# Kernel optimization log

Measured on AMD Instinct MI355X. Metric: run time of the kernel, lower is better.

Reference implementation:

```python
import jax, jax.numpy as jnp
import numpy as np

HIDDEN = 2048
INTER = 1408
N_ROUTED = 32
N_SHARED = 2
TOP_K = 6
B, S = 2, 1024


def setup_inputs() -> dict:
    key = jax.random.key(0)
    ks = jax.random.split(key, 9)
    scale = 0.02
    x = jax.random.normal(ks[0], (B, S, HIDDEN), dtype=jnp.float32)
    w_router = jax.random.normal(ks[1], (HIDDEN, N_ROUTED), dtype=jnp.float32) * scale
    wg = jax.random.normal(ks[2], (N_ROUTED, HIDDEN, INTER), dtype=jnp.float32) * scale
    wu = jax.random.normal(ks[3], (N_ROUTED, HIDDEN, INTER), dtype=jnp.float32) * scale
    wd = jax.random.normal(ks[4], (N_ROUTED, INTER, HIDDEN), dtype=jnp.float32) * scale
    sg = jax.random.normal(ks[5], (N_SHARED, HIDDEN, INTER), dtype=jnp.float32) * scale
    su = jax.random.normal(ks[6], (N_SHARED, HIDDEN, INTER), dtype=jnp.float32) * scale
    sd = jax.random.normal(ks[7], (N_SHARED, INTER, HIDDEN), dtype=jnp.float32) * scale
    return {"x": x, "w_router": w_router, "wg": wg, "wu": wu, "wd": wd,
            "sg": sg, "su": su, "sd": sd}


def _swiglu(xf, wg_e, wu_e, wd_e):
    # xf: [T, D]; wg_e/wu_e: [D, F]; wd_e: [F, D]
    h = jax.nn.silu(xf @ wg_e) * (xf @ wu_e)
    return h @ wd_e


def reference(x, w_router, wg, wu, wd, sg, su, sd):
    Bb, Ss, D = x.shape
    xf = x.reshape(-1, D)                      # [T, D], T = B*S
    T = xf.shape[0]

    # Shared experts: applied densely to every token, summed.
    shared = jnp.zeros_like(xf)
    for i in range(sg.shape[0]):               # small fixed count (2)
        shared = shared + _swiglu(xf, sg[i], su[i], sd[i])

    # Router: softmax over all routed experts, then top-k + renormalize.
    probs = jax.nn.softmax(xf @ w_router, axis=-1)            # [T, E]
    topw, topi = jax.lax.top_k(probs, TOP_K)                  # [T, K]
    topw = topw / jnp.sum(topw, axis=-1, keepdims=True)

    # Dense [T, E] combine weights (zero where expert not selected).
    E = wg.shape[0]
    wdense = jnp.zeros((T, E), dtype=xf.dtype)
    wdense = wdense.at[jnp.arange(T)[:, None], topi].add(topw)

    # Scan over experts, accumulating weighted expert outputs (memory-light).
    def body(acc, ew):
        wg_e, wu_e, wd_e, w_e = ew            # w_e: [T] combine weight for this expert
        y = _swiglu(xf, wg_e, wu_e, wd_e)     # [T, D]
        return acc + w_e[:, None] * y, None

    routed, _ = jax.lax.scan(body, jnp.zeros_like(xf), (wg, wu, wd, wdense.T))

    return (shared + routed).reshape(Bb, Ss, D)
```

## Files before the change

kernel.cpp:

```cpp
#include <hip/hip_runtime.h>
#include <hip/hip_bf16.h>

#define T_TOK 2048
#define D_HID 2048
#define F_INT 1408
#define N_EXP 32
#define TOPK 6
#define NJOBS 34
#define SH_BASE 12288
#define ROWS_TOTAL 16384
#define MAXT_GU 288
#define MAXT_DN 159
#define LDSW 40

typedef __bf16 bf16;
typedef __bf16 bf16x4 __attribute__((ext_vector_type(4)));
typedef __bf16 bf16x8 __attribute__((ext_vector_type(8)));
typedef float f32x4 __attribute__((ext_vector_type(4)));

#define BAR() asm volatile("s_waitcnt lgkmcnt(0)\n\ts_barrier" ::: "memory")

__device__ __forceinline__ int swz16(int r, int k) {
    return r * LDSW + (((k >> 3) ^ ((r >> 3) & 3)) << 3) + (k & 7);
}

__device__ __forceinline__ int decode_tile(const int* __restrict__ counts, int bid,
                                           int NBN, int MSH, int NSH,
                                           int& job, int& n0, int& m0) {
    int total = 0;
    for (int j = 0; j < NJOBS; ++j) {
        int c = (j < N_EXP) ? counts[j] : T_TOK;
        total += ((c + (1 << MSH) - 1) >> MSH) * NBN;
    }
    if (bid >= total) return 0;
    int q = total >> 3, r = total & 7, x = bid & 7, o = bid >> 3;
    int L = (x < r ? x * (q + 1) : r * (q + 1) + (x - r) * q) + o;
    int acc = 0;
    for (int j = 0; j < NJOBS; ++j) {
        int c = (j < N_EXP) ? counts[j] : T_TOK;
        int tc = (c + (1 << MSH) - 1) >> MSH;
        int b = tc * NBN;
        if (L < acc + b) {
            int rem = L - acc;
            int n0i = rem / tc;
            job = j;
            n0 = n0i << NSH;
            m0 = (rem - n0i * tc) << MSH;
            return 1;
        }
        acc += b;
    }
    return 0;
}

__global__ __launch_bounds__(256) void k_xcvt(const float* __restrict__ x,
                                              bf16* __restrict__ xb) {
    int i = blockIdx.x * 2048 + threadIdx.x * 8;
    float4 f0 = *(const float4*)(x + i);
    float4 f1 = *(const float4*)(x + i + 4);
    bf16x8 v = {(bf16)f0.x, (bf16)f0.y, (bf16)f0.z, (bf16)f0.w,
                (bf16)f1.x, (bf16)f1.y, (bf16)f1.z, (bf16)f1.w};
    *(bf16x8*)(xb + i) = v;
}

__global__ __launch_bounds__(256) void k_router(const float* __restrict__ x,
                                                const float* __restrict__ wr,
                                                int* __restrict__ counts,
                                                int* __restrict__ tok_e,
                                                float* __restrict__ tok_w) {
    int t = blockIdx.x;
    int tid = threadIdx.x;
    __shared__ float xs[D_HID];
    __shared__ float part[8][32];
    __shared__ float probs[N_EXP];

    const float4* xsrc = (const float4*)(x + (size_t)t * D_HID);
    float4* xdst = (float4*)xs;
    for (int i = tid; i < D_HID / 4; i += 256) xdst[i] = xsrc[i];
    __syncthreads();

    int e = tid & 31, c = tid >> 5;
    float p = 0.f;
    const float* wp = wr + e;
    #pragma unroll 8
    for (int h = c * 256; h < c * 256 + 256; ++h) p += xs[h] * wp[h * 32];
    part[c][e] = p;
    __syncthreads();

    if (tid < 32) {
        float l = 0.f;
        #pragma unroll
        for (int cc = 0; cc < 8; ++cc) l += part[cc][tid];
        float m = l;
        for (int off = 16; off; off >>= 1) m = fmaxf(m, __shfl_xor(m, off));
        float ex = __expf(l - m);
        float s = ex;
        for (int off = 16; off; off >>= 1) s += __shfl_xor(s, off);
        probs[tid] = ex / s;
    }
    __syncthreads();

    if (tid == 0) {
        unsigned used = 0;
        int ids[TOPK]; float wsv[TOPK]; float wsum = 0.f;
        for (int k = 0; k < TOPK; ++k) {
            int best = 0; float bv = -1.f;
            for (int ee = 0; ee < N_EXP; ++ee)
                if (!((used >> ee) & 1u) && probs[ee] > bv) { bv = probs[ee]; best = ee; }
            used |= 1u << best;
            ids[k] = best; wsv[k] = bv; wsum += bv;
        }
        float inv = 1.f / wsum;
        for (int k = 0; k < TOPK; ++k) {
            tok_e[t * TOPK + k] = ids[k];
            tok_w[t * TOPK + k] = wsv[k] * inv;
            atomicAdd(&counts[ids[k]], 1);
        }
    }
}

__global__ void k_plan(const int* __restrict__ counts, int* __restrict__ offs,
                       int* __restrict__ cursors) {
    int tid = threadIdx.x;
    if (tid < N_EXP) cursors[tid] = 0;
    if (tid == 0) {
        int o = 0;
        offs[0] = 0;
        for (int e2 = 0; e2 < N_EXP; ++e2) { o += counts[e2]; offs[e2 + 1] = o; }
        offs[33] = offs[32] + T_TOK;
        offs[34] = offs[33] + T_TOK;
    }
}

__global__ __launch_bounds__(256) void k_assign(const int* __restrict__ tok_e,
                                                const int* __restrict__ offs,
                                                int* __restrict__ cursors,
                                                int* __restrict__ slots,
                                                int* __restrict__ rowtok) {
    int t = blockIdx.x * 256 + threadIdx.x;
    #pragma unroll
    for (int k = 0; k < TOPK; ++k) {
        int e = tok_e[t * TOPK + k];
        int pos = atomicAdd(&cursors[e], 1);
        int slot = offs[e] + pos;
        slots[t * TOPK + k] = slot;
        rowtok[slot] = t;
    }
    rowtok[SH_BASE + t] = t;
    rowtok[SH_BASE + T_TOK + t] = t;
}

__global__ __launch_bounds__(256, 3) void k_gateup(
    const bf16* __restrict__ xb, const float* __restrict__ wg, const float* __restrict__ wu,
    const float* __restrict__ sg, const float* __restrict__ su,
    const int* __restrict__ rowtok, const int* __restrict__ counts, const int* __restrict__ offs,
    bf16* __restrict__ H) {

    int job, n0, m0;
    if (!decode_tile(counts, blockIdx.x, F_INT / 128, 6, 7, job, n0, m0)) return;
    int cnt = (job < N_EXP) ? counts[job] : T_TOK;
    int base = offs[job];
    const float* Wg = (job < N_EXP) ? wg + (size_t)job * D_HID * F_INT
                                    : sg + (size_t)(job - N_EXP) * D_HID * F_INT;
    const float* Wu = (job < N_EXP) ? wu + (size_t)job * D_HID * F_INT
                                    : su + (size_t)(job - N_EXP) * D_HID * F_INT;

    __shared__ bf16 As[2][64 * LDSW];
    __shared__ bf16 Bg[2][128 * LDSW];
    __shared__ bf16 Bu[2][128 * LDSW];

    int tid = threadIdx.x;
    int lane = tid & 63;
    int wid = tid >> 6;
    int wm = (wid >> 1) * 32;
    int wn = (wid & 1) * 64;

    int ar = tid >> 2;
    int akg = tid & 3;
    int grow_a = m0 + ar; if (grow_a > cnt - 1) grow_a = cnt - 1;
    const bf16* asrc = xb + (size_t)rowtok[base + grow_a] * D_HID + akg * 8;

    int k4 = (tid >> 5) * 4;
    int nn = (tid & 31) * 4;
    const float* gsrc = Wg + (size_t)k4 * F_INT + n0 + nn;
    const float* usrc = Wu + (size_t)k4 * F_INT + n0 + nn;

    f32x4 accg[2][4], accu[2][4];
    f32x4 zero = {0.f, 0.f, 0.f, 0.f};
    #pragma unroll
    for (int i = 0; i < 2; ++i)
        #pragma unroll
        for (int j = 0; j < 4; ++j) { accg[i][j] = zero; accu[i][j] = zero; }

    bf16x8 a_r8;
    float4 g_r[4], u_r[4];

    auto LOAD = [&](int k0) {
        a_r8 = *(const bf16x8*)(asrc + k0);
        const float* g0 = gsrc + (size_t)k0 * F_INT;
        g_r[0] = *(const float4*)g0;
        g_r[1] = *(const float4*)(g0 + F_INT);
        g_r[2] = *(const float4*)(g0 + 2 * F_INT);
        g_r[3] = *(const float4*)(g0 + 3 * F_INT);
        const float* u0 = usrc + (size_t)k0 * F_INT;
        u_r[0] = *(const float4*)u0;
        u_r[1] = *(const float4*)(u0 + F_INT);
        u_r[2] = *(const float4*)(u0 + 2 * F_INT);
        u_r[3] = *(const float4*)(u0 + 3 * F_INT);
    };

    auto WRITE = [&](int s) {
        *(bf16x8*)&As[s][swz16(ar, akg * 8)] = a_r8;
        bf16x4 p0 = {(bf16)g_r[0].x, (bf16)g_r[1].x, (bf16)g_r[2].x, (bf16)g_r[3].x};
        bf16x4 p1 = {(bf16)g_r[0].y, (bf16)g_r[1].y, (bf16)g_r[2].y, (bf16)g_r[3].y};
        bf16x4 p2 = {(bf16)g_r[0].z, (bf16)g_r[1].z, (bf16)g_r[2].z, (bf16)g_r[3].z};
        bf16x4 p3 = {(bf16)g_r[0].w, (bf16)g_r[1].w, (bf16)g_r[2].w, (bf16)g_r[3].w};
        *(bf16x4*)&Bg[s][swz16(nn + 0, k4)] = p0;
        *(bf16x4*)&Bg[s][swz16(nn + 1, k4)] = p1;
        *(bf16x4*)&Bg[s][swz16(nn + 2, k4)] = p2;
        *(bf16x4*)&Bg[s][swz16(nn + 3, k4)] = p3;
        bf16x4 q0 = {(bf16)u_r[0].x, (bf16)u_r[1].x, (bf16)u_r[2].x, (bf16)u_r[3].x};
        bf16x4 q1 = {(bf16)u_r[0].y, (bf16)u_r[1].y, (bf16)u_r[2].y, (bf16)u_r[3].y};
        bf16x4 q2 = {(bf16)u_r[0].z, (bf16)u_r[1].z, (bf16)u_r[2].z, (bf16)u_r[3].z};
        bf16x4 q3 = {(bf16)u_r[0].w, (bf16)u_r[1].w, (bf16)u_r[2].w, (bf16)u_r[3].w};
        *(bf16x4*)&Bu[s][swz16(nn + 0, k4)] = q0;
        *(bf16x4*)&Bu[s][swz16(nn + 1, k4)] = q1;
        *(bf16x4*)&Bu[s][swz16(nn + 2, k4)] = q2;
        *(bf16x4*)&Bu[s][swz16(nn + 3, k4)] = q3;
    };

    const int NT = D_HID / 32;
    LOAD(0);
    WRITE(0);
    LOAD(32);
    BAR();

    for (int kt = 0; kt < NT; ++kt) {
        int cur = kt & 1;
        if (kt + 1 < NT) WRITE(cur ^ 1);
        if (kt + 2 < NT) LOAD((kt + 2) * 32);

        int kgl = (lane >> 4) * 8;
        bf16x8 af[2];
        #pragma unroll
        for (int mf = 0; mf < 2; ++mf)
            af[mf] = *(const bf16x8*)&As[cur][swz16(wm + mf * 16 + (lane & 15), kgl)];
        #pragma unroll
        for (int nf = 0; nf < 4; ++nf) {
            int rn = wn + nf * 16 + (lane & 15);
            bf16x8 bfr = *(const bf16x8*)&Bg[cur][swz16(rn, kgl)];
            bf16x8 ufr = *(const bf16x8*)&Bu[cur][swz16(rn, kgl)];
            #pragma unroll
            for (int mf = 0; mf < 2; ++mf) {
                accg[mf][nf] = __builtin_amdgcn_mfma_f32_16x16x32_bf16(af[mf], bfr, accg[mf][nf], 0, 0, 0);
                accu[mf][nf] = __builtin_amdgcn_mfma_f32_16x16x32_bf16(af[mf], ufr, accu[mf][nf], 0, 0, 0);
            }
        }
        BAR();
    }

    #pragma unroll
    for (int mf = 0; mf < 2; ++mf) {
        #pragma unroll
        for (int nf = 0; nf < 4; ++nf) {
            int col = n0 + wn + nf * 16 + (lane & 15);
            #pragma unroll
            for (int r = 0; r < 4; ++r) {
                int grow = m0 + wm + mf * 16 + (lane >> 4) * 4 + r;
                if (grow < cnt) {
                    float g = accg[mf][nf][r];
                    float u = accu[mf][nf][r];
                    float h = g * u / (1.f + __expf(-g));
                    H[(size_t)(base + grow) * F_INT + col] = (bf16)h;
                }
            }
        }
    }
}

__global__ __launch_bounds__(256, 3) void k_down(
    const bf16* __restrict__ H, const float* __restrict__ wd, const float* __restrict__ sd,
    const int* __restrict__ counts, const int* __restrict__ offs,
    bf16* __restrict__ P) {

    int job, n0, m0;
    if (!decode_tile(counts, blockIdx.x, D_HID / 128, 7, 7, job, n0, m0)) return;
    int cnt = (job < N_EXP) ? counts[job] : T_TOK;
    int base = offs[job];
    const float* Wd = (job < N_EXP) ? wd + (size_t)job * F_INT * D_HID
                                    : sd + (size_t)(job - N_EXP) * F_INT * D_HID;

    __shared__ bf16 As[2][128 * LDSW];
    __shared__ bf16 Bs[2][128 * LDSW];

    int tid = threadIdx.x;
    int lane = tid & 63;
    int wid = tid >> 6;
    int wm = (wid >> 1) * 64;
    int wn = (wid & 1) * 64;

    int ar = tid >> 1;
    int akg2 = (tid & 1) * 2;
    int grow_a = m0 + ar; if (grow_a > cnt - 1) grow_a = cnt - 1;
    const bf16* asrc = H + (size_t)(base + grow_a) * F_INT + akg2 * 8;

    int k4 = (tid >> 5) * 4;
    int nn = (tid & 31) * 4;
    const float* bsrc = Wd + (size_t)k4 * D_HID + n0 + nn;

    f32x4 acc[4][4];
    f32x4 zero = {0.f, 0.f, 0.f, 0.f};
    #pragma unroll
    for (int i = 0; i < 4; ++i)
        #pragma unroll
        for (int j = 0; j < 4; ++j) acc[i][j] = zero;

    bf16x8 h_r[2];
    float4 b_r[4];

    auto LOAD = [&](int k0) {
        h_r[0] = *(const bf16x8*)(asrc + k0);
        h_r[1] = *(const bf16x8*)(asrc + k0 + 8);
        const float* b0 = bsrc + (size_t)k0 * D_HID;
        b_r[0] = *(const float4*)b0;
        b_r[1] = *(const float4*)(b0 + D_HID);
        b_r[2] = *(const float4*)(b0 + 2 * D_HID);
        b_r[3] = *(const float4*)(b0 + 3 * D_HID);
    };

    auto WRITE = [&](int s) {
        *(bf16x8*)&As[s][swz16(ar, akg2 * 8)] = h_r[0];
        *(bf16x8*)&As[s][swz16(ar, (akg2 + 1) * 8)] = h_r[1];
        bf16x4 p0 = {(bf16)b_r[0].x, (bf16)b_r[1].x, (bf16)b_r[2].x, (bf16)b_r[3].x};
        bf16x4 p1 = {(bf16)b_r[0].y, (bf16)b_r[1].y, (bf16)b_r[2].y, (bf16)b_r[3].y};
        bf16x4 p2 = {(bf16)b_r[0].z, (bf16)b_r[1].z, (bf16)b_r[2].z, (bf16)b_r[3].z};
        bf16x4 p3 = {(bf16)b_r[0].w, (bf16)b_r[1].w, (bf16)b_r[2].w, (bf16)b_r[3].w};
        *(bf16x4*)&Bs[s][swz16(nn + 0, k4)] = p0;
        *(bf16x4*)&Bs[s][swz16(nn + 1, k4)] = p1;
        *(bf16x4*)&Bs[s][swz16(nn + 2, k4)] = p2;
        *(bf16x4*)&Bs[s][swz16(nn + 3, k4)] = p3;
    };

    const int NT = F_INT / 32;
    LOAD(0);
    WRITE(0);
    LOAD(32);
    BAR();

    for (int kt = 0; kt < NT; ++kt) {
        int cur = kt & 1;
        if (kt + 1 < NT) WRITE(cur ^ 1);
        if (kt + 2 < NT) LOAD((kt + 2) * 32);

        int kgl = (lane >> 4) * 8;
        bf16x8 af[4];
        #pragma unroll
        for (int mf = 0; mf < 4; ++mf)
            af[mf] = *(const bf16x8*)&As[cur][swz16(wm + mf * 16 + (lane & 15), kgl)];
        #pragma unroll
        for (int nf = 0; nf < 4; ++nf) {
            int rn = wn + nf * 16 + (lane & 15);
            bf16x8 bfr = *(const bf16x8*)&Bs[cur][swz16(rn, kgl)];
            #pragma unroll
            for (int mf = 0; mf < 4; ++mf)
                acc[mf][nf] = __builtin_amdgcn_mfma_f32_16x16x32_bf16(af[mf], bfr, acc[mf][nf], 0, 0, 0);
        }
        BAR();
    }

    #pragma unroll
    for (int mf = 0; mf < 4; ++mf) {
        #pragma unroll
        for (int nf = 0; nf < 4; ++nf) {
            int col = n0 + wn + nf * 16 + (lane & 15);
            #pragma unroll
            for (int r = 0; r < 4; ++r) {
                int grow = m0 + wm + mf * 16 + (lane >> 4) * 4 + r;
                if (grow < cnt)
                    P[(size_t)(base + grow) * D_HID + col] = (bf16)acc[mf][nf][r];
            }
        }
    }
}

__global__ __launch_bounds__(256) void k_combine(const bf16* __restrict__ P,
                                                 const int* __restrict__ slots,
                                                 const float* __restrict__ tok_w,
                                                 float* __restrict__ out) {
    int t = blockIdx.x;
    int tid = threadIdx.x;
    __shared__ int ss[TOPK];
    __shared__ float ww[TOPK];
    if (tid < TOPK) { ss[tid] = slots[t * TOPK + tid]; ww[tid] = tok_w[t * TOPK + tid]; }
    __syncthreads();
    int c0 = tid * 8;
    float acc[8];
    {
        bf16x8 v0 = *(const bf16x8*)(P + (size_t)(SH_BASE + t) * D_HID + c0);
        bf16x8 v1 = *(const bf16x8*)(P + (size_t)(SH_BASE + T_TOK + t) * D_HID + c0);
        #pragma unroll
        for (int i = 0; i < 8; ++i) acc[i] = (float)v0[i] + (float)v1[i];
    }
    #pragma unroll
    for (int k = 0; k < TOPK; ++k) {
        bf16x8 v = *(const bf16x8*)(P + (size_t)ss[k] * D_HID + c0);
        float w = ww[k];
        #pragma unroll
        for (int i = 0; i < 8; ++i) acc[i] += w * (float)v[i];
    }
    float4 o0 = {acc[0], acc[1], acc[2], acc[3]};
    float4 o1 = {acc[4], acc[5], acc[6], acc[7]};
    *(float4*)(out + (size_t)t * D_HID + c0) = o0;
    *(float4*)(out + (size_t)t * D_HID + c0 + 4) = o1;
}

extern "C" void kernel_launch(void* const* d_in, const int* in_sizes, int n_in,
                              void* d_out, int out_size, void* d_ws, size_t ws_size,
                              hipStream_t stream) {
    const float* x  = (const float*)d_in[0];
    const float* wr = (const float*)d_in[1];
    const float* wg = (const float*)d_in[2];
    const float* wu = (const float*)d_in[3];
    const float* wd = (const float*)d_in[4];
    const float* sg = (const float*)d_in[5];
    const float* su = (const float*)d_in[6];
    const float* sd = (const float*)d_in[7];
    float* out = (float*)d_out;

    char* w = (char*)d_ws;
    int*   counts   = (int*)(w + 0);
    int*   cursors  = (int*)(w + 256);
    int*   offs     = (int*)(w + 512);
    int*   tok_e    = (int*)(w + 8192);
    float* tok_w    = (float*)(w + 8192 + 49152);
    int*   slots    = (int*)(w + 8192 + 2 * 49152);
    int*   rowtok   = (int*)(w + 8192 + 3 * 49152);
    bf16*  H        = (bf16*)(w + 262144);
    bf16*  P        = (bf16*)(w + 262144 + (size_t)ROWS_TOTAL * F_INT * 2);
    bf16*  Xb       = (bf16*)(w + 262144 + (size_t)ROWS_TOTAL * F_INT * 2
                                        + (size_t)ROWS_TOTAL * D_HID * 2);

    hipMemsetAsync(counts, 0, 128, stream);
    k_xcvt<<<T_TOK * D_HID / 2048, 256, 0, stream>>>(x, Xb);
    k_router<<<T_TOK, 256, 0, stream>>>(x, wr, counts, tok_e, tok_w);
    k_plan<<<1, 64, 0, stream>>>(counts, offs, cursors);
    k_assign<<<T_TOK / 256, 256, 0, stream>>>(tok_e, offs, cursors, slots, rowtok);
    k_gateup<<<MAXT_GU * (F_INT / 128), 256, 0, stream>>>(
        Xb, wg, wu, sg, su, rowtok, counts, offs, H);
    k_down<<<MAXT_DN * (D_HID / 128), 256, 0, stream>>>(
        H, wd, sd, counts, offs, P);
    k_combine<<<T_TOK, 256, 0, stream>>>(P, slots, tok_w, out);
}
```

Before: 777.1 us.

## Retile gate/up GEMM to 256-row tiles with gate/up wave specialization

```diff
diff --git a/kernel.cpp b/kernel.cpp
--- a/kernel.cpp
+++ b/kernel.cpp
@@ -9,7 +9,8 @@
 #define NJOBS 34
 #define SH_BASE 12288
 #define ROWS_TOTAL 16384
-#define MAXT_GU 288
+#define MAXT_GU 96
+#define GU_NBN 22
 #define MAXT_DN 159
 #define LDSW 40
 
@@ -24,13 +25,12 @@
     return r * LDSW + (((k >> 3) ^ ((r >> 3) & 3)) << 3) + (k & 7);
 }
 
-__device__ __forceinline__ int decode_tile(const int* __restrict__ counts, int bid,
-                                           int NBN, int MSH, int NSH,
-                                           int& job, int& n0, int& m0) {
+__device__ __forceinline__ int decode_gu(const int* __restrict__ counts, int bid,
+                                         int& job, int& n0, int& m0) {
     int total = 0;
     for (int j = 0; j < NJOBS; ++j) {
         int c = (j < N_EXP) ? counts[j] : T_TOK;
-        total += ((c + (1 << MSH) - 1) >> MSH) * NBN;
+        total += ((c + 255) >> 8) * GU_NBN;
     }
     if (bid >= total) return 0;
     int q = total >> 3, r = total & 7, x = bid & 7, o = bid >> 3;
@@ -38,14 +38,42 @@
     int acc = 0;
     for (int j = 0; j < NJOBS; ++j) {
         int c = (j < N_EXP) ? counts[j] : T_TOK;
-        int tc = (c + (1 << MSH) - 1) >> MSH;
+        int tc = (c + 255) >> 8;
+        int b = tc * GU_NBN;
+        if (L < acc + b) {
+            int rem = L - acc;
+            job = j;
+            m0 = (rem / GU_NBN) << 8;
+            n0 = (rem % GU_NBN) << 6;
+            return 1;
+        }
+        acc += b;
+    }
+    return 0;
+}
+
+__device__ __forceinline__ int decode_dn(const int* __restrict__ counts, int bid,
+                                         int& job, int& n0, int& m0) {
+    const int NBN = D_HID / 128;
+    int total = 0;
+    for (int j = 0; j < NJOBS; ++j) {
+        int c = (j < N_EXP) ? counts[j] : T_TOK;
+        total += ((c + 127) >> 7) * NBN;
+    }
+    if (bid >= total) return 0;
+    int q = total >> 3, r = total & 7, x = bid & 7, o = bid >> 3;
+    int L = (x < r ? x * (q + 1) : r * (q + 1) + (x - r) * q) + o;
+    int acc = 0;
+    for (int j = 0; j < NJOBS; ++j) {
+        int c = (j < N_EXP) ? counts[j] : T_TOK;
+        int tc = (c + 127) >> 7;
         int b = tc * NBN;
         if (L < acc + b) {
             int rem = L - acc;
             int n0i = rem / tc;
             job = j;
-            n0 = n0i << NSH;
-            m0 = (rem - n0i * tc) << MSH;
+            n0 = n0i << 7;
+            m0 = (rem - n0i * tc) << 7;
             return 1;
         }
         acc += b;
@@ -150,14 +178,14 @@
     rowtok[SH_BASE + T_TOK + t] = t;
 }
 
-__global__ __launch_bounds__(256, 3) void k_gateup(
+__global__ __launch_bounds__(512, 4) void k_gateup(
     const bf16* __restrict__ xb, const float* __restrict__ wg, const float* __restrict__ wu,
     const float* __restrict__ sg, const float* __restrict__ su,
     const int* __restrict__ rowtok, const int* __restrict__ counts, const int* __restrict__ offs,
     bf16* __restrict__ H) {
 
     int job, n0, m0;
-    if (!decode_tile(counts, blockIdx.x, F_INT / 128, 6, 7, job, n0, m0)) return;
+    if (!decode_gu(counts, blockIdx.x, job, n0, m0)) return;
     int cnt = (job < N_EXP) ? counts[job] : T_TOK;
     int base = offs[job];
     const float* Wg = (job < N_EXP) ? wg + (size_t)job * D_HID * F_INT
@@ -165,68 +193,68 @@
     const float* Wu = (job < N_EXP) ? wu + (size_t)job * D_HID * F_INT
                                     : su + (size_t)(job - N_EXP) * D_HID * F_INT;
 
-    __shared__ bf16 As[2][64 * LDSW];
-    __shared__ bf16 Bg[2][128 * LDSW];
-    __shared__ bf16 Bu[2][128 * LDSW];
+    __shared__ bf16 AsF[2 * 256 * LDSW];
+    __shared__ bf16 BgF[2 * 64 * LDSW];
+    __shared__ bf16 BuF[2 * 64 * LDSW];
 
     int tid = threadIdx.x;
     int lane = tid & 63;
     int wid = tid >> 6;
-    int wm = (wid >> 1) * 32;
-    int wn = (wid & 1) * 64;
-
-    int ar = tid >> 2;
-    int akg = tid & 3;
+    int mat = wid & 1;
+    int wm = (wid >> 1) * 64;
+
+    int bt  = tid & 127;
+    int kk  = (bt >> 4) * 4;
+    int nn  = (bt & 15) * 4;
+    const float* wsrc = ((wid < 2) ? Wg : Wu) + (size_t)kk * F_INT + n0 + nn;
+    bf16* bdst = (wid < 2) ? BgF : BuF;
+    int ar = tid & 255;
     int grow_a = m0 + ar; if (grow_a > cnt - 1) grow_a = cnt - 1;
-    const bf16* asrc = xb + (size_t)rowtok[base + grow_a] * D_HID + akg * 8;
-
-    int k4 = (tid >> 5) * 4;
-    int nn = (tid & 31) * 4;
-    const float* gsrc = Wg + (size_t)k4 * F_INT + n0 + nn;
-    const float* usrc = Wu + (size_t)k4 * F_INT + n0 + nn;
-
-    f32x4 accg[2][4], accu[2][4];
+    const bf16* asrc = xb + (size_t)rowtok[base + grow_a] * D_HID;
+
+    f32x4 acc[4][4];
     f32x4 zero = {0.f, 0.f, 0.f, 0.f};
     #pragma unroll
-    for (int i = 0; i < 2; ++i)
-        #pragma unroll
-        for (int j = 0; j < 4; ++j) { accg[i][j] = zero; accu[i][j] = zero; }
-
-    bf16x8 a_r8;
-    float4 g_r[4], u_r[4];
+    for (int i = 0; i < 4; ++i)
+        #pragma unroll
+        for (int j = 0; j < 4; ++j) acc[i][j] = zero;
+
+    float4 st[4];
 
     auto LOAD = [&](int k0) {
-        a_r8 = *(const bf16x8*)(asrc + k0);
-        const float* g0 = gsrc + (size_t)k0 * F_INT;
-        g_r[0] = *(const float4*)g0;
-        g_r[1] = *(const float4*)(g0 + F_INT);
-        g_r[2] = *(const float4*)(g0 + 2 * F_INT);
-        g_r[3] = *(const float4*)(g0 + 3 * F_INT);
-        const float* u0 = usrc + (size_t)k0 * F_INT;
-        u_r[0] = *(const float4*)u0;
-        u_r[1] = *(const float4*)(u0 + F_INT);
-        u_r[2] = *(const float4*)(u0 + 2 * F_INT);
-        u_r[3] = *(const float4*)(u0 + 3 * F_INT);
+        if (wid < 4) {
+            const float* s0 = wsrc + (size_t)k0 * F_INT;
+            st[0] = *(const float4*)s0;
+            st[1] = *(const float4*)(s0 + F_INT);
+            st[2] = *(const float4*)(s0 + 2 * F_INT);
+            st[3] = *(const float4*)(s0 + 3 * F_INT);
+        } else {
+            const bf16* a0 = asrc + k0;
+            st[0] = *(const float4*)(const void*)(a0);
+            st[1] = *(const float4*)(const void*)(a0 + 8);
+            st[2] = *(const float4*)(const void*)(a0 + 16);
+            st[3] = *(const float4*)(const void*)(a0 + 24);
+        }
     };
 
     auto WRITE = [&](int s) {
-        *(bf16x8*)&As[s][swz16(ar, akg * 8)] = a_r8;
-        bf16x4 p0 = {(bf16)g_r[0].x, (bf16)g_r[1].x, (bf16)g_r[2].x, (bf16)g_r[3].x};
-        bf16x4 p1 = {(bf16)g_r[0].y, (bf16)g_r[1].y, (bf16)g_r[2].y, (bf16)g_r[3].y};
-        bf16x4 p2 = {(bf16)g_r[0].z, (bf16)g_r[1].z, (bf16)g_r[2].z, (bf16)g_r[3].z};
-        bf16x4 p3 = {(bf16)g_r[0].w, (bf16)g_r[1].w, (bf16)g_r[2].w, (bf16)g_r[3].w};
-        *(bf16x4*)&Bg[s][swz16(nn + 0, k4)] = p0;
-        *(bf16x4*)&Bg[s][swz16(nn + 1, k4)] = p1;
-        *(bf16x4*)&Bg[s][swz16(nn + 2, k4)] = p2;
-        *(bf16x4*)&Bg[s][swz16(nn + 3, k4)] = p3;
-        bf16x4 q0 = {(bf16)u_r[0].x, (bf16)u_r[1].x, (bf16)u_r[2].x, (bf16)u_r[3].x};
-        bf16x4 q1 = {(bf16)u_r[0].y, (bf16)u_r[1].y, (bf16)u_r[2].y, (bf16)u_r[3].y};
-        bf16x4 q2 = {(bf16)u_r[0].z, (bf16)u_r[1].z, (bf16)u_r[2].z, (bf16)u_r[3].z};
-        bf16x4 q3 = {(bf16)u_r[0].w, (bf16)u_r[1].w, (bf16)u_r[2].w, (bf16)u_r[3].w};
-        *(bf16x4*)&Bu[s][swz16(nn + 0, k4)] = q0;
-        *(bf16x4*)&Bu[s][swz16(nn + 1, k4)] = q1;
-        *(bf16x4*)&Bu[s][swz16(nn + 2, k4)] = q2;
-        *(bf16x4*)&Bu[s][swz16(nn + 3, k4)] = q3;
+        if (wid < 4) {
+            bf16* bd = bdst + s * (64 * LDSW);
+            bf16x4 p0 = {(bf16)st[0].x, (bf16)st[1].x, (bf16)st[2].x, (bf16)st[3].x};
+            bf16x4 p1 = {(bf16)st[0].y, (bf16)st[1].y, (bf16)st[2].y, (bf16)st[3].y};
+            bf16x4 p2 = {(bf16)st[0].z, (bf16)st[1].z, (bf16)st[2].z, (bf16)st[3].z};
+            bf16x4 p3 = {(bf16)st[0].w, (bf16)st[1].w, (bf16)st[2].w, (bf16)st[3].w};
+            *(bf16x4*)&bd[swz16(nn + 0, kk)] = p0;
+            *(bf16x4*)&bd[swz16(nn + 1, kk)] = p1;
+            *(bf16x4*)&bd[swz16(nn + 2, kk)] = p2;
+            *(bf16x4*)&bd[swz16(nn + 3, kk)] = p3;
+        } else {
+            bf16* ad = AsF + s * (256 * LDSW);
+            *(float4*)(void*)&ad[swz16(ar, 0)]  = st[0];
+            *(float4*)(void*)&ad[swz16(ar, 8)]  = st[1];
+            *(float4*)(void*)&ad[swz16(ar, 16)] = st[2];
+            *(float4*)(void*)&ad[swz16(ar, 24)] = st[3];
+        }
     };
 
     const int NT = D_HID / 32;
@@ -235,46 +263,60 @@
     LOAD(32);
     BAR();
 
+    const bf16* bread = mat ? BuF : BgF;
     for (int kt = 0; kt < NT; ++kt) {
         int cur = kt & 1;
         if (kt + 1 < NT) WRITE(cur ^ 1);
         if (kt + 2 < NT) LOAD((kt + 2) * 32);
 
         int kgl = (lane >> 4) * 8;
-        bf16x8 af[2];
-        #pragma unroll
-        for (int mf = 0; mf < 2; ++mf)
-            af[mf] = *(const bf16x8*)&As[cur][swz16(wm + mf * 16 + (lane & 15), kgl)];
+        const bf16* ac = AsF + cur * (256 * LDSW);
+        const bf16* bc = bread + cur * (64 * LDSW);
+        bf16x8 af[4];
+        #pragma unroll
+        for (int mf = 0; mf < 4; ++mf)
+            af[mf] = *(const bf16x8*)&ac[swz16(wm + mf * 16 + (lane & 15), kgl)];
         #pragma unroll
         for (int nf = 0; nf < 4; ++nf) {
-            int rn = wn + nf * 16 + (lane & 15);
-            bf16x8 bfr = *(const bf16x8*)&Bg[cur][swz16(rn, kgl)];
-            bf16x8 ufr = *(const bf16x8*)&Bu[cur][swz16(rn, kgl)];
+            bf16x8 bfr = *(const bf16x8*)&bc[swz16(nf * 16 + (lane & 15), kgl)];
             #pragma unroll
-            for (int mf = 0; mf < 2; ++mf) {
-                accg[mf][nf] = __builtin_amdgcn_mfma_f32_16x16x32_bf16(af[mf], bfr, accg[mf][nf], 0, 0, 0);
-                accu[mf][nf] = __builtin_amdgcn_mfma_f32_16x16x32_bf16(af[mf], ufr, accu[mf][nf], 0, 0, 0);
-            }
+            for (int mf = 0; mf < 4; ++mf)
+                acc[mf][nf] = __builtin_amdgcn_mfma_f32_16x16x32_bf16(af[mf], bfr, acc[mf][nf], 0, 0, 0);
         }
         BAR();
     }
 
-    #pragma unroll
-    for (int mf = 0; mf < 2; ++mf) {
-        #pragma unroll
-        for (int nf = 0; nf < 4; ++nf) {
-            int col = n0 + wn + nf * 16 + (lane & 15);
+    bf16* uscr = AsF;
+    if (mat == 1) {
+        #pragma unroll
+        for (int mf = 0; mf < 4; ++mf)
             #pragma unroll
-            for (int r = 0; r < 4; ++r) {
-                int grow = m0 + wm + mf * 16 + (lane >> 4) * 4 + r;
-                if (grow < cnt) {
-                    float g = accg[mf][nf][r];
-                    float u = accu[mf][nf][r];
-                    float h = g * u / (1.f + __expf(-g));
-                    H[(size_t)(base + grow) * F_INT + col] = (bf16)h;
+            for (int nf = 0; nf < 4; ++nf)
+                #pragma unroll
+                for (int r = 0; r < 4; ++r) {
+                    int row = mf * 16 + (lane >> 4) * 4 + r;
+                    int col = nf * 16 + (lane & 15);
+                    uscr[(wm + row) * 64 + (col ^ ((row & 7) << 3))] = (bf16)acc[mf][nf][r];
                 }
-            }
-        }
+    }
+    __syncthreads();
+    if (mat == 0) {
+        #pragma unroll
+        for (int mf = 0; mf < 4; ++mf)
+            #pragma unroll
+            for (int nf = 0; nf < 4; ++nf)
+                #pragma unroll
+                for (int r = 0; r < 4; ++r) {
+                    int row = mf * 16 + (lane >> 4) * 4 + r;
+                    int col = nf * 16 + (lane & 15);
+                    int grow = m0 + wm + row;
+                    if (grow < cnt) {
+                        float u = (float)uscr[(wm + row) * 64 + (col ^ ((row & 7) << 3))];
+                        float g = acc[mf][nf][r];
+                        float h = g * u / (1.f + __expf(-g));
+                        H[(size_t)(base + grow) * F_INT + n0 + col] = (bf16)h;
+                    }
+                }
     }
 }
 
@@ -284,7 +326,7 @@
     bf16* __restrict__ P) {
 
     int job, n0, m0;
-    if (!decode_tile(counts, blockIdx.x, D_HID / 128, 7, 7, job, n0, m0)) return;
+    if (!decode_dn(counts, blockIdx.x, job, n0, m0)) return;
     int cnt = (job < N_EXP) ? counts[job] : T_TOK;
     int base = offs[job];
     const float* Wd = (job < N_EXP) ? wd + (size_t)job * F_INT * D_HID
@@ -445,7 +487,7 @@
     k_router<<<T_TOK, 256, 0, stream>>>(x, wr, counts, tok_e, tok_w);
     k_plan<<<1, 64, 0, stream>>>(counts, offs, cursors);
     k_assign<<<T_TOK / 256, 256, 0, stream>>>(tok_e, offs, cursors, slots, rowtok);
-    k_gateup<<<MAXT_GU * (F_INT / 128), 256, 0, stream>>>(
+    k_gateup<<<MAXT_GU * GU_NBN, 512, 0, stream>>>(
         Xb, wg, wu, sg, su, rowtok, counts, offs, H);
     k_down<<<MAXT_DN * (D_HID / 128), 256, 0, stream>>>(
         H, wd, sd, counts, offs, P);
```

After: 1.179 ms. +51.8%, slower.

## Reshape gate/up tile to 128 tokens by 64 columns and extend LDS swizzle

Applied to the files above, without the earlier changes.

```diff
diff --git a/kernel.cpp b/kernel.cpp
--- a/kernel.cpp
+++ b/kernel.cpp
@@ -9,7 +9,8 @@
 #define NJOBS 34
 #define SH_BASE 12288
 #define ROWS_TOTAL 16384
-#define MAXT_GU 288
+#define MAXT_GU 159
+#define GU_NBN 22
 #define MAXT_DN 159
 #define LDSW 40
 
@@ -21,7 +22,7 @@
 #define BAR() asm volatile("s_waitcnt lgkmcnt(0)\n\ts_barrier" ::: "memory")
 
 __device__ __forceinline__ int swz16(int r, int k) {
-    return r * LDSW + (((k >> 3) ^ ((r >> 3) & 3)) << 3) + (k & 7);
+    return r * LDSW + ((((k >> 3) ^ ((r >> 3) & 3) ^ ((r >> 5) & 3)) & 3) << 3) + (k & 7);
 }
 
 __device__ __forceinline__ int decode_tile(const int* __restrict__ counts, int bid,
@@ -157,7 +158,7 @@
     bf16* __restrict__ H) {
 
     int job, n0, m0;
-    if (!decode_tile(counts, blockIdx.x, F_INT / 128, 6, 7, job, n0, m0)) return;
+    if (!decode_tile(counts, blockIdx.x, GU_NBN, 7, 6, job, n0, m0)) return;
     int cnt = (job < N_EXP) ? counts[job] : T_TOK;
     int base = offs[job];
     const float* Wg = (job < N_EXP) ? wg + (size_t)job * D_HID * F_INT
@@ -165,68 +166,58 @@
     const float* Wu = (job < N_EXP) ? wu + (size_t)job * D_HID * F_INT
                                     : su + (size_t)(job - N_EXP) * D_HID * F_INT;
 
-    __shared__ bf16 As[2][64 * LDSW];
-    __shared__ bf16 Bg[2][128 * LDSW];
-    __shared__ bf16 Bu[2][128 * LDSW];
+    __shared__ bf16 As[2][128 * LDSW];
+    __shared__ bf16 Bg[2][64 * LDSW];
+    __shared__ bf16 Bu[2][64 * LDSW];
 
     int tid = threadIdx.x;
     int lane = tid & 63;
     int wid = tid >> 6;
-    int wm = (wid >> 1) * 32;
-    int wn = (wid & 1) * 64;
-
-    int ar = tid >> 2;
-    int akg = tid & 3;
+    int wm = (wid & 1) * 64;
+    int wn = (wid >> 1) * 32;
+
+    int ar = tid >> 1;
+    int akg2 = (tid & 1) * 2;
     int grow_a = m0 + ar; if (grow_a > cnt - 1) grow_a = cnt - 1;
-    const bf16* asrc = xb + (size_t)rowtok[base + grow_a] * D_HID + akg * 8;
-
-    int k4 = (tid >> 5) * 4;
-    int nn = (tid & 31) * 4;
-    const float* gsrc = Wg + (size_t)k4 * F_INT + n0 + nn;
-    const float* usrc = Wu + (size_t)k4 * F_INT + n0 + nn;
-
-    f32x4 accg[2][4], accu[2][4];
+    const bf16* asrc = xb + (size_t)rowtok[base + grow_a] * D_HID + akg2 * 8;
+
+    int sub = tid & 127;
+    int k4 = (sub & 7) * 4;
+    int nn = (sub >> 3) * 4;
+    const float* wsrc = ((tid & 128) ? Wu : Wg) + (size_t)k4 * F_INT + n0 + nn;
+
+    f32x4 accg[4][2], accu[4][2];
     f32x4 zero = {0.f, 0.f, 0.f, 0.f};
     #pragma unroll
-    for (int i = 0; i < 2; ++i)
-        #pragma unroll
-        for (int j = 0; j < 4; ++j) { accg[i][j] = zero; accu[i][j] = zero; }
-
-    bf16x8 a_r8;
-    float4 g_r[4], u_r[4];
+    for (int i = 0; i < 4; ++i)
+        #pragma unroll
+        for (int j = 0; j < 2; ++j) { accg[i][j] = zero; accu[i][j] = zero; }
+
+    bf16x8 a_r[2];
+    float4 b_r[4];
 
     auto LOAD = [&](int k0) {
-        a_r8 = *(const bf16x8*)(asrc + k0);
-        const float* g0 = gsrc + (size_t)k0 * F_INT;
-        g_r[0] = *(const float4*)g0;
-        g_r[1] = *(const float4*)(g0 + F_INT);
-        g_r[2] = *(const float4*)(g0 + 2 * F_INT);
-        g_r[3] = *(const float4*)(g0 + 3 * F_INT);
-        const float* u0 = usrc + (size_t)k0 * F_INT;
-        u_r[0] = *(const float4*)u0;
-        u_r[1] = *(const float4*)(u0 + F_INT);
-        u_r[2] = *(const float4*)(u0 + 2 * F_INT);
-        u_r[3] = *(const float4*)(u0 + 3 * F_INT);
+        a_r[0] = *(const bf16x8*)(asrc + k0);
+        a_r[1] = *(const bf16x8*)(asrc + k0 + 8);
+        const float* b0 = wsrc + (size_t)k0 * F_INT;
+        b_r[0] = *(const float4*)b0;
+        b_r[1] = *(const float4*)(b0 + F_INT);
+        b_r[2] = *(const float4*)(b0 + 2 * F_INT);
+        b_r[3] = *(const float4*)(b0 + 3 * F_INT);
     };
 
     auto WRITE = [&](int s) {
-        *(bf16x8*)&As[s][swz16(ar, akg * 8)] = a_r8;
-        bf16x4 p0 = {(bf16)g_r[0].x, (bf16)g_r[1].x, (bf16)g_r[2].x, (bf16)g_r[3].x};
-        bf16x4 p1 = {(bf16)g_r[0].y, (bf16)g_r[1].y, (bf16)g_r[2].y, (bf16)g_r[3].y};
-        bf16x4 p2 = {(bf16)g_r[0].z, (bf16)g_r[1].z, (bf16)g_r[2].z, (bf16)g_r[3].z};
-        bf16x4 p3 = {(bf16)g_r[0].w, (bf16)g_r[1].w, (bf16)g_r[2].w, (bf16)g_r[3].w};
-        *(bf16x4*)&Bg[s][swz16(nn + 0, k4)] = p0;
-        *(bf16x4*)&Bg[s][swz16(nn + 1, k4)] = p1;
-        *(bf16x4*)&Bg[s][swz16(nn + 2, k4)] = p2;
-        *(bf16x4*)&Bg[s][swz16(nn + 3, k4)] = p3;
-        bf16x4 q0 = {(bf16)u_r[0].x, (bf16)u_r[1].x, (bf16)u_r[2].x, (bf16)u_r[3].x};
-        bf16x4 q1 = {(bf16)u_r[0].y, (bf16)u_r[1].y, (bf16)u_r[2].y, (bf16)u_r[3].y};
-        bf16x4 q2 = {(bf16)u_r[0].z, (bf16)u_r[1].z, (bf16)u_r[2].z, (bf16)u_r[3].z};
-        bf16x4 q3 = {(bf16)u_r[0].w, (bf16)u_r[1].w, (bf16)u_r[2].w, (bf16)u_r[3].w};
-        *(bf16x4*)&Bu[s][swz16(nn + 0, k4)] = q0;
-        *(bf16x4*)&Bu[s][swz16(nn + 1, k4)] = q1;
-        *(bf16x4*)&Bu[s][swz16(nn + 2, k4)] = q2;
-        *(bf16x4*)&Bu[s][swz16(nn + 3, k4)] = q3;
+        *(bf16x8*)&As[s][swz16(ar, akg2 * 8)] = a_r[0];
+        *(bf16x8*)&As[s][swz16(ar, (akg2 + 1) * 8)] = a_r[1];
+        bf16* bd = (tid & 128) ? Bu[s] : Bg[s];
+        bf16x4 p0 = {(bf16)b_r[0].x, (bf16)b_r[1].x, (bf16)b_r[2].x, (bf16)b_r[3].x};
+        bf16x4 p1 = {(bf16)b_r[0].y, (bf16)b_r[1].y, (bf16)b_r[2].y, (bf16)b_r[3].y};
+        bf16x4 p2 = {(bf16)b_r[0].z, (bf16)b_r[1].z, (bf16)b_r[2].z, (bf16)b_r[3].z};
+        bf16x4 p3 = {(bf16)b_r[0].w, (bf16)b_r[1].w, (bf16)b_r[2].w, (bf16)b_r[3].w};
+        *(bf16x4*)&bd[swz16(nn + 0, k4)] = p0;
+        *(bf16x4*)&bd[swz16(nn + 1, k4)] = p1;
+        *(bf16x4*)&bd[swz16(nn + 2, k4)] = p2;
+        *(bf16x4*)&bd[swz16(nn + 3, k4)] = p3;
     };
 
     const int NT = D_HID / 32;
@@ -241,17 +232,18 @@
         if (kt + 2 < NT) LOAD((kt + 2) * 32);
 
         int kgl = (lane >> 4) * 8;
-        bf16x8 af[2];
-        #pragma unroll
-        for (int mf = 0; mf < 2; ++mf)
+        bf16x8 af[4];
+        #pragma unroll
+        for (int mf = 0; mf < 4; ++mf)
             af[mf] = *(const bf16x8*)&As[cur][swz16(wm + mf * 16 + (lane & 15), kgl)];
         #pragma unroll
-        for (int nf = 0; nf < 4; ++nf) {
+        for (int nf = 0; nf < 2; ++nf) {
             int rn = wn + nf * 16 + (lane & 15);
-            bf16x8 bfr = *(const bf16x8*)&Bg[cur][swz16(rn, kgl)];
-            bf16x8 ufr = *(const bf16x8*)&Bu[cur][swz16(rn, kgl)];
+            int o = swz16(rn, kgl);
+            bf16x8 bfr = *(const bf16x8*)&Bg[cur][o];
+            bf16x8 ufr = *(const bf16x8*)&Bu[cur][o];
             #pragma unroll
-            for (int mf = 0; mf < 2; ++mf) {
+            for (int mf = 0; mf < 4; ++mf) {
                 accg[mf][nf] = __builtin_amdgcn_mfma_f32_16x16x32_bf16(af[mf], bfr, accg[mf][nf], 0, 0, 0);
                 accu[mf][nf] = __builtin_amdgcn_mfma_f32_16x16x32_bf16(af[mf], ufr, accu[mf][nf], 0, 0, 0);
             }
@@ -260,9 +252,9 @@
     }
 
     #pragma unroll
-    for (int mf = 0; mf < 2; ++mf) {
-        #pragma unroll
-        for (int nf = 0; nf < 4; ++nf) {
+    for (int mf = 0; mf < 4; ++mf) {
+        #pragma unroll
+        for (int nf = 0; nf < 2; ++nf) {
             int col = n0 + wn + nf * 16 + (lane & 15);
             #pragma unroll
             for (int r = 0; r < 4; ++r) {
@@ -445,7 +437,7 @@
     k_router<<<T_TOK, 256, 0, stream>>>(x, wr, counts, tok_e, tok_w);
     k_plan<<<1, 64, 0, stream>>>(counts, offs, cursors);
     k_assign<<<T_TOK / 256, 256, 0, stream>>>(tok_e, offs, cursors, slots, rowtok);
-    k_gateup<<<MAXT_GU * (F_INT / 128), 256, 0, stream>>>(
+    k_gateup<<<MAXT_GU * GU_NBN, 256, 0, stream>>>(
         Xb, wg, wu, sg, su, rowtok, counts, offs, H);
     k_down<<<MAXT_DN * (D_HID / 128), 256, 0, stream>>>(
         H, wd, sd, counts, offs, P);
```

Measured after the change: 888.6 us. 14.3% more time.
